# Optimization experiments

Measured on AMD Instinct MI355X. Metric: run time of the kernel, lower is better.

The kernel has to match this reference:

```python
import jax, jax.numpy as jnp
import numpy as np

EPS = 1e-5
NH, NP = 12, 4  # heads, points per level


def _ln(x, g, b):
    m = x.mean(-1, keepdims=True)
    v = x.var(-1, keepdims=True)
    return (x - m) / jnp.sqrt(v + EPS) * g + b


def _bilinear(v, g, H_, W_):
    # v: [B, nh, H_*W_, d] flattened feature map; g: [B, nh, Lq, np, 2] normalized locs in [0,1]
    # torch grid_sample(align_corners=False, padding='zeros') with grid = 2*loc-1 => pixel = loc*W - 0.5
    x = g[..., 0] * W_ - 0.5
    y = g[..., 1] * H_ - 0.5
    x0 = jnp.floor(x)
    y0 = jnp.floor(y)
    wx1 = x - x0
    wy1 = y - y0
    wx0 = 1.0 - wx1
    wy0 = 1.0 - wy1
    d = v.shape[-1]
    Bn, nh, Lq, np_ = x.shape
    out = jnp.zeros((Bn, nh, Lq, np_, d), v.dtype)
    for xi, yi, w in ((x0, y0, wx0 * wy0), (x0 + 1, y0, wx1 * wy0),
                      (x0, y0 + 1, wx0 * wy1), (x0 + 1, y0 + 1, wx1 * wy1)):
        valid = (xi >= 0) & (xi < W_) & (yi >= 0) & (yi < H_)
        xc = jnp.clip(xi, 0, W_ - 1).astype(jnp.int32)
        yc = jnp.clip(yi, 0, H_ - 1).astype(jnp.int32)
        idx = (yc * W_ + xc).reshape(Bn, nh, Lq * np_, 1)
        gv = jnp.take_along_axis(v, idx, axis=2).reshape(Bn, nh, Lq, np_, d)
        out = out + (w * valid.astype(v.dtype))[..., None] * gv
    return out


def setup_inputs() -> dict:
    key = jax.random.key(0)
    ks = jax.random.split(key, 16)
    B, Lq, C = 4, 4096, 768
    nl = 1
    Hs = Ws = 64
    Lin = Hs * Ws
    hid = int(C * 0.25)
    s = 0.02
    f32 = jnp.float32
    return {
        'query': jax.random.normal(ks[0], (B, Lq, C), f32),
        'reference_points': jax.random.uniform(ks[1], (B, Lq, nl, 2), f32),
        'feat': jax.random.normal(ks[2], (B, Lin, C), f32),
        'spatial_shapes': np.array([[Hs, Ws]], dtype=np.int64),
        'level_start_index': np.array([0], dtype=np.int64),
        'H': Hs, 'W': Ws,
        'qn_g': jnp.ones(C, f32), 'qn_b': jnp.zeros(C, f32),
        'fn_g': jnp.ones(C, f32), 'fn_b': jnp.zeros(C, f32),
        'Wv': jax.random.normal(ks[3], (C, C), f32) * s, 'bv': jnp.zeros(C, f32),
        'Woff': jax.random.normal(ks[4], (C, NH * nl * NP * 2), f32) * s,
        'boff': jax.random.normal(ks[5], (NH * nl * NP * 2,), f32) * 0.1,
        'Watt': jax.random.normal(ks[6], (C, NH * nl * NP), f32) * s,
        'batt': jnp.zeros(NH * nl * NP, f32),
        'Wout': jax.random.normal(ks[7], (C, C), f32) * s, 'bout': jnp.zeros(C, f32),
        'ffn_g': jnp.ones(C, f32), 'ffn_b': jnp.zeros(C, f32),
        'W1': jax.random.normal(ks[8], (C, hid), f32) * s, 'b1': jnp.zeros(hid, f32),
        'W2': jax.random.normal(ks[9], (hid, C), f32) * s, 'b2': jnp.zeros(C, f32),
    }


def reference(query, reference_points, feat, spatial_shapes, level_start_index, H, W,
              qn_g, qn_b, fn_g, fn_b, Wv, bv, Woff, boff, Watt, batt, Wout, bout,
              ffn_g, ffn_b, W1, b1, W2, b2):
    B, Lq, C = query.shape
    nl = spatial_shapes.shape[0]
    d = C // NH
    qn = _ln(query, qn_g, qn_b)
    fn = _ln(feat, fn_g, fn_b)
    value = (fn @ Wv + bv).reshape(B, -1, NH, d)
    off = (qn @ Woff + boff).reshape(B, Lq, NH, nl, NP, 2)
    attw = jax.nn.softmax((qn @ Watt + batt).reshape(B, Lq, NH, nl * NP), axis=-1)
    attw = attw.reshape(B, Lq, NH, nl, NP)
    # offset normalizer is [W_l, H_l]
    norm = np.stack([spatial_shapes[:, 1], spatial_shapes[:, 0]], -1).astype(np.float32)
    loc = reference_points[:, :, None, :, None, :] + off / jnp.asarray(norm)[None, None, None, :, None, :]
    out = jnp.zeros((B, NH, Lq, d), query.dtype)
    for l in range(nl):
        H_, W_ = int(spatial_shapes[l, 0]), int(spatial_shapes[l, 1])
        s0 = int(level_start_index[l])
        v = value[:, s0:s0 + H_ * W_].transpose(0, 2, 1, 3)       # [B, nh, HW, d]
        g = loc[:, :, :, l].transpose(0, 2, 1, 3, 4)              # [B, nh, Lq, np, 2]
        sampled = _bilinear(v, g, H_, W_)                         # [B, nh, Lq, np, d]
        w = attw[:, :, :, l].transpose(0, 2, 1, 3)                # [B, nh, Lq, np]
        out = out + jnp.sum(sampled * w[..., None], axis=3)
    attn = out.transpose(0, 2, 1, 3).reshape(B, Lq, C) @ Wout + bout
    query = query + attn
    h = _ln(query, ffn_g, ffn_b)
    h = jax.nn.gelu(h @ W1 + b1, approximate=False)
    return query + (h @ W2 + b2)
```

## Files before the change

kernel.cpp:

```cpp
#include <hip/hip_runtime.h>
#include <hip/hip_bf16.h>
#include <math.h>

#define B_    4
#define LQ    4096
#define CC    768
#define NH_   12
#define DH    64
#define NP_   4
#define HH    64
#define WW    64
#define HID   192
#define ROWS  (B_ * LQ)
#define EPS_  1e-5f

typedef __bf16 bf16x8 __attribute__((ext_vector_type(8)));
typedef __bf16 bf16x4 __attribute__((ext_vector_type(4)));
typedef float  f32x4  __attribute__((ext_vector_type(4)));

typedef __attribute__((address_space(3))) void* lds_vp;
typedef const __attribute__((address_space(1))) void* gbl_vp;

struct PrepJob { const float* W; __bf16* Wt; int K; int N; int Npad; };
struct PrepJobs { PrepJob j[6]; };

__global__ __launch_bounds__(256)
void prep_all(PrepJobs jobs) {
    PrepJob job = jobs.j[blockIdx.z];
    int k0 = blockIdx.x * 64, n0 = blockIdx.y * 64;
    if (k0 >= job.K || n0 >= job.Npad) return;
    __shared__ float tile[64][65];
    int c = threadIdx.x & 63, r0 = threadIdx.x >> 6;
    #pragma unroll
    for (int i = 0; i < 16; ++i) {
        int kk = i * 4 + r0;
        float v = 0.f;
        if (k0 + kk < job.K && n0 + c < job.N) v = job.W[(size_t)(k0 + kk) * job.N + n0 + c];
        tile[kk][c] = v;
    }
    __syncthreads();
    #pragma unroll
    for (int i = 0; i < 16; ++i) {
        int nn = i * 4 + r0;
        if (n0 + nn < job.Npad && k0 + c < job.K)
            job.Wt[(size_t)(n0 + nn) * job.K + k0 + c] = (__bf16)tile[c][nn];
    }
}

__inline__ __device__ float wave_sum64(float v) {
    #pragma unroll
    for (int o = 32; o > 0; o >>= 1) v += __shfl_down(v, o, 64);
    return v;
}

__global__ __launch_bounds__(256)
void ln2_kernel(const float* __restrict__ x0, const float* __restrict__ g0,
                const float* __restrict__ b0, __bf16* __restrict__ y0,
                const float* __restrict__ x1, const float* __restrict__ g1,
                const float* __restrict__ b1, __bf16* __restrict__ y1) {
    int sel = blockIdx.y;
    const float* x = sel ? x1 : x0;
    const float* g = sel ? g1 : g0;
    const float* b = sel ? b1 : b0;
    __bf16* y = sel ? y1 : y0;
    int row = blockIdx.x;
    const float* xr = x + (size_t)row * CC;
    __bf16* yr = y + (size_t)row * CC;
    int t = threadIdx.x;
    f32x4 xv = {0.f, 0.f, 0.f, 0.f};
    if (t < 192) xv = *(const f32x4*)(xr + t * 4);
    float s  = xv[0] + xv[1] + xv[2] + xv[3];
    float s2 = xv[0]*xv[0] + xv[1]*xv[1] + xv[2]*xv[2] + xv[3]*xv[3];
    __shared__ float red[8];
    float ws = wave_sum64(s), ws2 = wave_sum64(s2);
    int w = t >> 6;
    if ((t & 63) == 0) { red[w] = ws; red[4 + w] = ws2; }
    __syncthreads();
    float S  = red[0] + red[1] + red[2] + red[3];
    float S2 = red[4] + red[5] + red[6] + red[7];
    float mean = S / CC;
    float inv  = rsqrtf(S2 / CC - mean * mean + EPS_);
    if (t < 192) {
        f32x4 gv = *(const f32x4*)(g + t * 4);
        f32x4 bv = *(const f32x4*)(b + t * 4);
        bf16x4 o;
        #pragma unroll
        for (int e = 0; e < 4; ++e)
            o[e] = (__bf16)((xv[e] - mean) * inv * gv[e] + bv[e]);
        *(bf16x4*)(yr + t * 4) = o;
    }
}

__global__ __launch_bounds__(256)
void ln_bf_kernel(const __bf16* __restrict__ x, const float* __restrict__ g,
                  const float* __restrict__ b, __bf16* __restrict__ y) {
    int row = blockIdx.x;
    const __bf16* xr = x + (size_t)row * CC;
    __bf16* yr = y + (size_t)row * CC;
    int t = threadIdx.x;
    float xv[8]; bf16x8 raw = {};
    if (t < 96) raw = *(const bf16x8*)(xr + t * 8);
    float s = 0.f, s2 = 0.f;
    #pragma unroll
    for (int e = 0; e < 8; ++e) { xv[e] = (float)raw[e]; s += xv[e]; s2 += xv[e]*xv[e]; }
    __shared__ float red[8];
    float ws = wave_sum64(s), ws2 = wave_sum64(s2);
    int w = t >> 6;
    if ((t & 63) == 0) { red[w] = ws; red[4 + w] = ws2; }
    __syncthreads();
    float S  = red[0] + red[1] + red[2] + red[3];
    float S2 = red[4] + red[5] + red[6] + red[7];
    float mean = S / CC;
    float inv  = rsqrtf(S2 / CC - mean * mean + EPS_);
    if (t < 96) {
        bf16x8 o;
        #pragma unroll
        for (int e = 0; e < 8; ++e)
            o[e] = (__bf16)((xv[e] - mean) * inv * g[t * 8 + e] + b[t * 8 + e]);
        *(bf16x8*)(yr + t * 8) = o;
    }
}

__global__ __launch_bounds__(256)
void gemm_bt(const __bf16* __restrict__ A, const __bf16* __restrict__ Bt,
             const float* __restrict__ ba, int Nsplit, const float* __restrict__ bb,
             const void* __restrict__ res, void* __restrict__ out,
             int M, int K, int N, int flags) {
    __shared__ __bf16 As[128 * 32];
    __shared__ __bf16 Bs[128 * 32];

    int t = threadIdx.x;
    int lane = t & 63, wave = t >> 6;
    int bm = blockIdx.y * 128, bn = blockIdx.x * 128;
    int wm = wave & 1, wn = wave >> 1;

    f32x4 acc[4][4] = {};

    int row0 = t >> 2,           kc0 = (t & 3) ^ ((row0 >> 1) & 3);
    int row1 = (256 + t) >> 2,   kc1 = ((256 + t) & 3) ^ ((row1 >> 1) & 3);

    const __bf16* a0 = A  + (size_t)(bm + row0) * K + kc0 * 8;
    const __bf16* a1 = A  + (size_t)(bm + row1) * K + kc1 * 8;
    const __bf16* b0 = Bt + (size_t)(bn + row0) * K + kc0 * 8;
    const __bf16* b1 = Bt + (size_t)(bn + row1) * K + kc1 * 8;

    int rbase = wm * 64 + (lane & 15);
    int nbase = wn * 64 + (lane & 15);
    int kq = lane >> 4;

    for (int k0 = 0; k0 < K; k0 += 32) {
        __syncthreads();
        __builtin_amdgcn_global_load_lds((gbl_vp)(a0 + k0), (lds_vp)&As[t * 8], 16, 0, 0);
        __builtin_amdgcn_global_load_lds((gbl_vp)(a1 + k0), (lds_vp)&As[(256 + t) * 8], 16, 0, 0);
        __builtin_amdgcn_global_load_lds((gbl_vp)(b0 + k0), (lds_vp)&Bs[t * 8], 16, 0, 0);
        __builtin_amdgcn_global_load_lds((gbl_vp)(b1 + k0), (lds_vp)&Bs[(256 + t) * 8], 16, 0, 0);
        __syncthreads();

        bf16x8 afr[4], bfr[4];
        #pragma unroll
        for (int i = 0; i < 4; ++i) {
            int r = rbase + i * 16;
            afr[i] = *(const bf16x8*)&As[r * 32 + ((kq ^ ((r >> 1) & 3)) * 8)];
        }
        #pragma unroll
        for (int j = 0; j < 4; ++j) {
            int n = nbase + j * 16;
            bfr[j] = *(const bf16x8*)&Bs[n * 32 + ((kq ^ ((n >> 1) & 3)) * 8)];
        }
        #pragma unroll
        for (int i = 0; i < 4; ++i)
            #pragma unroll
            for (int j = 0; j < 4; ++j)
                acc[i][j] = __builtin_amdgcn_mfma_f32_16x16x32_bf16(afr[i], bfr[j], acc[i][j], 0, 0, 0);
    }

    int rowq = lane >> 4;
    int colj[4]; float biasj[4];
    #pragma unroll
    for (int j = 0; j < 4; ++j) {
        int c = bn + wn * 64 + j * 16 + (lane & 15);
        colj[j] = c;
        biasj[j] = (c < N) ? ((c < Nsplit) ? ba[c] : bb[c - Nsplit]) : 0.f;
    }
    int do_gelu = flags & 1, out_bf = flags & 2, res_bf = flags & 4;
    #pragma unroll
    for (int i = 0; i < 4; ++i) {
        #pragma unroll
        for (int r = 0; r < 4; ++r) {
            int m = bm + wm * 64 + i * 16 + rowq * 4 + r;
            #pragma unroll
            for (int j = 0; j < 4; ++j) {
                if (colj[j] < N) {
                    float v = acc[i][j][r] + biasj[j];
                    if (do_gelu) v = 0.5f * v * (1.f + erff(v * 0.70710678118f));
                    size_t oi = (size_t)m * N + colj[j];
                    if (res) v += res_bf ? (float)((const __bf16*)res)[oi]
                                         : ((const float*)res)[oi];
                    if (out_bf) ((__bf16*)out)[oi] = (__bf16)v;
                    else        ((float*)out)[oi]  = v;
                }
            }
        }
    }
}

__global__ __launch_bounds__(256)
void gemm_bt64(const __bf16* __restrict__ A, const __bf16* __restrict__ Bt,
               const float* __restrict__ ba, int Nsplit, const float* __restrict__ bb,
               void* __restrict__ out, int M, int K, int N, int flags) {
    __shared__ __bf16 As[64 * 32];
    __shared__ __bf16 Bs[64 * 32];

    int t = threadIdx.x;
    int lane = t & 63, wave = t >> 6;
    int bm = blockIdx.y * 64, bn = blockIdx.x * 64;

    f32x4 acc[4] = {};

    int row0 = t >> 2, kc0 = (t & 3) ^ ((row0 >> 1) & 3);
    const __bf16* a0 = A  + (size_t)(bm + row0) * K + kc0 * 8;
    const __bf16* b0 = Bt + (size_t)(bn + row0) * K + kc0 * 8;

    int rbase = wave * 16 + (lane & 15);
    int nbase = lane & 15;
    int kq = lane >> 4;

    for (int k0 = 0; k0 < K; k0 += 32) {
        __syncthreads();
        __builtin_amdgcn_global_load_lds((gbl_vp)(a0 + k0), (lds_vp)&As[t * 8], 16, 0, 0);
        __builtin_amdgcn_global_load_lds((gbl_vp)(b0 + k0), (lds_vp)&Bs[t * 8], 16, 0, 0);
        __syncthreads();

        bf16x8 afr = *(const bf16x8*)&As[rbase * 32 + ((kq ^ ((rbase >> 1) & 3)) * 8)];
        #pragma unroll
        for (int j = 0; j < 4; ++j) {
            int n = nbase + j * 16;
            bf16x8 bfr = *(const bf16x8*)&Bs[n * 32 + ((kq ^ ((n >> 1) & 3)) * 8)];
            acc[j] = __builtin_amdgcn_mfma_f32_16x16x32_bf16(afr, bfr, acc[j], 0, 0, 0);
        }
    }

    int rowq = lane >> 4;
    int do_gelu = flags & 1, out_bf = flags & 2;
    #pragma unroll
    for (int r = 0; r < 4; ++r) {
        int m = bm + wave * 16 + rowq * 4 + r;
        #pragma unroll
        for (int j = 0; j < 4; ++j) {
            int c = bn + j * 16 + (lane & 15);
            if (c < N) {
                float v = acc[j][r] + ((c < Nsplit) ? ba[c] : bb[c - Nsplit]);
                if (do_gelu) v = 0.5f * v * (1.f + erff(v * 0.70710678118f));
                size_t oi = (size_t)m * N + c;
                if (out_bf) ((__bf16*)out)[oi] = (__bf16)v;
                else        ((float*)out)[oi]  = v;
            }
        }
    }
}

__global__ __launch_bounds__(256)
void sample_kernel(const __bf16* __restrict__ value, const float* __restrict__ offatt,
                   const float* __restrict__ refp, __bf16* __restrict__ out) {
    int wid  = blockIdx.x * 4 + (threadIdx.x >> 6);
    int lane = threadIdx.x & 63;
    int h  = wid % NH_;
    int bq = wid / NH_;
    int b  = bq / LQ;

    const float* oa = offatt + (size_t)bq * 144;
    float rx = refp[(size_t)bq * 2 + 0] * (float)WW - 0.5f;
    float ry = refp[(size_t)bq * 2 + 1] * (float)HH - 0.5f;

    float l0 = oa[96 + h * 4 + 0], l1 = oa[96 + h * 4 + 1];
    float l2 = oa[96 + h * 4 + 2], l3 = oa[96 + h * 4 + 3];
    float mx = fmaxf(fmaxf(l0, l1), fmaxf(l2, l3));
    float e0 = __expf(l0 - mx), e1 = __expf(l1 - mx);
    float e2 = __expf(l2 - mx), e3 = __expf(l3 - mx);
    float rs = 1.f / (e0 + e1 + e2 + e3);

    int pp = lane >> 4;
    int g  = lane & 15;
    float wpl = (pp == 0) ? e0 : (pp == 1) ? e1 : (pp == 2) ? e2 : e3;
    wpl *= rs;

    const float* oxy = oa + h * 8 + pp * 2;
    float x = rx + oxy[0];
    float y = ry + oxy[1];
    float x0f = floorf(x), y0f = floorf(y);
    float wx1 = x - x0f, wy1 = y - y0f;
    float wx0 = 1.f - wx1, wy0 = 1.f - wy1;
    int x0 = (int)x0f, y0 = (int)y0f;
    int x1 = x0 + 1, y1 = y0 + 1;
    float mx0 = ((unsigned)x0 < (unsigned)WW) ? wx0 : 0.f;
    float mx1 = ((unsigned)x1 < (unsigned)WW) ? wx1 : 0.f;
    float my0 = (((unsigned)y0 < (unsigned)HH) ? wy0 : 0.f) * wpl;
    float my1 = (((unsigned)y1 < (unsigned)HH) ? wy1 : 0.f) * wpl;
    int xc0 = x0 & (WW - 1), xc1 = x1 & (WW - 1);
    int r0 = (y0 & (HH - 1)) << 6, r1 = (y1 & (HH - 1)) << 6;

    const __bf16* vbase = value + (size_t)b * (LQ * CC) + h * DH + g * 4;
    bf16x4 v00 = *(const bf16x4*)(vbase + (size_t)(r0 + xc0) * CC);
    bf16x4 v01 = *(const bf16x4*)(vbase + (size_t)(r0 + xc1) * CC);
    bf16x4 v10 = *(const bf16x4*)(vbase + (size_t)(r1 + xc0) * CC);
    bf16x4 v11 = *(const bf16x4*)(vbase + (size_t)(r1 + xc1) * CC);
    float w00 = mx0 * my0, w01 = mx1 * my0, w10 = mx0 * my1, w11 = mx1 * my1;

    f32x4 acc;
    #pragma unroll
    for (int e = 0; e < 4; ++e)
        acc[e] = w00 * (float)v00[e] + w01 * (float)v01[e]
               + w10 * (float)v10[e] + w11 * (float)v11[e];

    #pragma unroll
    for (int e = 0; e < 4; ++e) {
        acc[e] += __shfl_xor(acc[e], 16, 64);
        acc[e] += __shfl_xor(acc[e], 32, 64);
    }
    if (pp == 0) {
        bf16x4 o;
        o[0] = (__bf16)acc[0]; o[1] = (__bf16)acc[1];
        o[2] = (__bf16)acc[2]; o[3] = (__bf16)acc[3];
        *(bf16x4*)(out + (size_t)bq * CC + h * DH + g * 4) = o;
    }
}

extern "C" void kernel_launch(void* const* d_in, const int* in_sizes, int n_in,
                              void* d_out, int out_size, void* d_ws, size_t ws_size,
                              hipStream_t stream) {
    const float* query = (const float*)d_in[0];
    const float* refp  = (const float*)d_in[1];
    const float* feat  = (const float*)d_in[2];
    const float* qn_g  = (const float*)d_in[7];
    const float* qn_b  = (const float*)d_in[8];
    const float* fn_g  = (const float*)d_in[9];
    const float* fn_b  = (const float*)d_in[10];
    const float* Wv    = (const float*)d_in[11];
    const float* bv    = (const float*)d_in[12];
    const float* Woff  = (const float*)d_in[13];
    const float* boff  = (const float*)d_in[14];
    const float* Watt  = (const float*)d_in[15];
    const float* batt  = (const float*)d_in[16];
    const float* Wout  = (const float*)d_in[17];
    const float* bout  = (const float*)d_in[18];
    const float* ffn_g = (const float*)d_in[19];
    const float* ffn_b = (const float*)d_in[20];
    const float* W1    = (const float*)d_in[21];
    const float* b1    = (const float*)d_in[22];
    const float* W2    = (const float*)d_in[23];
    const float* b2    = (const float*)d_in[24];
    float* out = (float*)d_out;

    char* ws = (char*)d_ws;
    __bf16* WvT    = (__bf16*)(ws + 0);
    __bf16* WcombT = (__bf16*)(ws + 1179648);
    __bf16* WoutT  = (__bf16*)(ws + 1572864);
    __bf16* W1T    = (__bf16*)(ws + 2752512);
    __bf16* W2T    = (__bf16*)(ws + 3145728);
    float*  offatt_f = (float*)(ws + 3670016);
    __bf16* h1_bf    = (__bf16*)offatt_f;
    __bf16* bufA     = (__bf16*)(ws + 13107200);
    __bf16* qn_bf    = bufA;
    __bf16* value_bf = bufA;
    __bf16* bufB     = (__bf16*)(ws + 38273024);
    __bf16* fn_bf    = bufB;
    __bf16* samp_bf  = bufB;
    __bf16* h_bf     = bufB;
    __bf16* attn_bf  = (__bf16*)(ws + 63438848);

    dim3 blk(256);

    PrepJobs jobs;
    jobs.j[0] = {Wv,   WvT,             768, 768, 768};
    jobs.j[1] = {Woff, WcombT,          768,  96,  96};
    jobs.j[2] = {Watt, WcombT + 96*768, 768,  48,  96};
    jobs.j[3] = {Wout, WoutT,           768, 768, 768};
    jobs.j[4] = {W1,   W1T,             768, 192, 192};
    jobs.j[5] = {W2,   W2T,             192, 768, 768};
    prep_all<<<dim3(12, 12, 6), blk, 0, stream>>>(jobs);

    ln2_kernel<<<dim3(ROWS, 2), blk, 0, stream>>>(query, qn_g, qn_b, qn_bf,
                                                  feat,  fn_g, fn_b, fn_bf);

    gemm_bt64<<<dim3(3, ROWS / 64), blk, 0, stream>>>(
        qn_bf, WcombT, boff, 96, batt, offatt_f, ROWS, CC, 144, 0);
    gemm_bt<<<dim3(6, ROWS / 128), blk, 0, stream>>>(
        fn_bf, WvT, bv, CC, nullptr, nullptr, value_bf, ROWS, CC, CC, 2);
    sample_kernel<<<ROWS * NH_ / 4, blk, 0, stream>>>(value_bf, offatt_f, refp, samp_bf);
    gemm_bt<<<dim3(6, ROWS / 128), blk, 0, stream>>>(
        samp_bf, WoutT, bout, CC, nullptr, query, attn_bf, ROWS, CC, CC, 2);
    ln_bf_kernel<<<ROWS, blk, 0, stream>>>(attn_bf, ffn_g, ffn_b, h_bf);
    gemm_bt64<<<dim3(3, ROWS / 64), blk, 0, stream>>>(
        h_bf, W1T, b1, HID, nullptr, h1_bf, ROWS, CC, HID, 1 | 2);
    gemm_bt<<<dim3(6, ROWS / 128), blk, 0, stream>>>(
        h1_bf, W2T, b2, CC, nullptr, attn_bf, out, ROWS, HID, CC, 4);
}
```

Measured before the change: 451.3 us.

## Triple-buffer GEMM LDS tiles with async prefetch and swizzle block order

```diff
diff --git a/kernel.cpp b/kernel.cpp
--- a/kernel.cpp
+++ b/kernel.cpp
@@ -126,12 +126,19 @@
              const float* __restrict__ ba, int Nsplit, const float* __restrict__ bb,
              const void* __restrict__ res, void* __restrict__ out,
              int M, int K, int N, int flags) {
-    __shared__ __bf16 As[128 * 32];
-    __shared__ __bf16 Bs[128 * 32];
+    __shared__ __bf16 As[3][128 * 32];
+    __shared__ __bf16 Bs[3][128 * 32];
 
     int t = threadIdx.x;
     int lane = t & 63, wave = t >> 6;
-    int bm = blockIdx.y * 128, bn = blockIdx.x * 128;
+
+    int nwg = gridDim.x * gridDim.y;
+    int bid = blockIdx.y * gridDim.x + blockIdx.x;
+    int cpx = nwg >> 3;
+    int swz = (bid & 7) * cpx + (bid >> 3);
+    int bx = swz % gridDim.x, by = swz / gridDim.x;
+    int bm = by * 128, bn = bx * 128;
+
     int wm = wave & 1, wn = wave >> 1;
 
     f32x4 acc[4][4] = {};
@@ -148,31 +155,54 @@
     int nbase = wn * 64 + (lane & 15);
     int kq = lane >> 4;
 
-    for (int k0 = 0; k0 < K; k0 += 32) {
-        __syncthreads();
-        __builtin_amdgcn_global_load_lds((gbl_vp)(a0 + k0), (lds_vp)&As[t * 8], 16, 0, 0);
-        __builtin_amdgcn_global_load_lds((gbl_vp)(a1 + k0), (lds_vp)&As[(256 + t) * 8], 16, 0, 0);
-        __builtin_amdgcn_global_load_lds((gbl_vp)(b0 + k0), (lds_vp)&Bs[t * 8], 16, 0, 0);
-        __builtin_amdgcn_global_load_lds((gbl_vp)(b1 + k0), (lds_vp)&Bs[(256 + t) * 8], 16, 0, 0);
-        __syncthreads();
-
-        bf16x8 afr[4], bfr[4];
-        #pragma unroll
-        for (int i = 0; i < 4; ++i) {
-            int r = rbase + i * 16;
-            afr[i] = *(const bf16x8*)&As[r * 32 + ((kq ^ ((r >> 1) & 3)) * 8)];
-        }
-        #pragma unroll
-        for (int j = 0; j < 4; ++j) {
-            int n = nbase + j * 16;
-            bfr[j] = *(const bf16x8*)&Bs[n * 32 + ((kq ^ ((n >> 1) & 3)) * 8)];
-        }
-        #pragma unroll
-        for (int i = 0; i < 4; ++i)
-            #pragma unroll
-            for (int j = 0; j < 4; ++j)
-                acc[i][j] = __builtin_amdgcn_mfma_f32_16x16x32_bf16(afr[i], bfr[j], acc[i][j], 0, 0, 0);
-    }
+    #define STAGE128(bi, kt) do {                                                              \
+        int koff_ = (kt) * 32;                                                                 \
+        __builtin_amdgcn_global_load_lds((gbl_vp)(a0 + koff_), (lds_vp)&As[bi][t * 8], 16, 0, 0);         \
+        __builtin_amdgcn_global_load_lds((gbl_vp)(a1 + koff_), (lds_vp)&As[bi][(256 + t) * 8], 16, 0, 0); \
+        __builtin_amdgcn_global_load_lds((gbl_vp)(b0 + koff_), (lds_vp)&Bs[bi][t * 8], 16, 0, 0);         \
+        __builtin_amdgcn_global_load_lds((gbl_vp)(b1 + koff_), (lds_vp)&Bs[bi][(256 + t) * 8], 16, 0, 0); \
+    } while (0)
+
+    #define COMPUTE128(bi) do {                                                                \
+        bf16x8 afr[4], bfr[4];                                                                 \
+        _Pragma("unroll")                                                                      \
+        for (int i = 0; i < 4; ++i) {                                                          \
+            int r = rbase + i * 16;                                                            \
+            afr[i] = *(const bf16x8*)&As[bi][r * 32 + ((kq ^ ((r >> 1) & 3)) * 8)];            \
+        }                                                                                      \
+        _Pragma("unroll")                                                                      \
+        for (int j = 0; j < 4; ++j) {                                                          \
+            int n = nbase + j * 16;                                                            \
+            bfr[j] = *(const bf16x8*)&Bs[bi][n * 32 + ((kq ^ ((n >> 1) & 3)) * 8)];            \
+        }                                                                                      \
+        _Pragma("unroll")                                                                      \
+        for (int i = 0; i < 4; ++i)                                                            \
+            _Pragma("unroll")                                                                  \
+            for (int j = 0; j < 4; ++j)                                                        \
+                acc[i][j] = __builtin_amdgcn_mfma_f32_16x16x32_bf16(afr[i], bfr[j], acc[i][j], 0, 0, 0); \
+    } while (0)
+
+    int nt = K >> 5;
+    STAGE128(0, 0);
+    STAGE128(1, 1);
+    int bi = 0;
+    for (int tt = 0; tt < nt - 2; ++tt) {
+        int bnxt = bi + 2; if (bnxt >= 3) bnxt -= 3;
+        STAGE128(bnxt, tt + 2);
+        asm volatile("s_waitcnt vmcnt(8)\n\ts_barrier" ::: "memory");
+        COMPUTE128(bi);
+        asm volatile("s_barrier" ::: "memory");
+        ++bi; if (bi >= 3) bi -= 3;
+    }
+    asm volatile("s_waitcnt vmcnt(4)\n\ts_barrier" ::: "memory");
+    COMPUTE128(bi);
+    asm volatile("s_barrier" ::: "memory");
+    ++bi; if (bi >= 3) bi -= 3;
+    asm volatile("s_waitcnt vmcnt(0)\n\ts_barrier" ::: "memory");
+    COMPUTE128(bi);
+
+    #undef STAGE128
+    #undef COMPUTE128
 
     int rowq = lane >> 4;
     int colj[4]; float biasj[4];
@@ -208,12 +238,18 @@
 void gemm_bt64(const __bf16* __restrict__ A, const __bf16* __restrict__ Bt,
                const float* __restrict__ ba, int Nsplit, const float* __restrict__ bb,
                void* __restrict__ out, int M, int K, int N, int flags) {
-    __shared__ __bf16 As[64 * 32];
-    __shared__ __bf16 Bs[64 * 32];
+    __shared__ __bf16 As[3][64 * 32];
+    __shared__ __bf16 Bs[3][64 * 32];
 
     int t = threadIdx.x;
     int lane = t & 63, wave = t >> 6;
-    int bm = blockIdx.y * 64, bn = blockIdx.x * 64;
+
+    int nwg = gridDim.x * gridDim.y;
+    int bid = blockIdx.y * gridDim.x + blockIdx.x;
+    int cpx = nwg >> 3;
+    int swz = (bid & 7) * cpx + (bid >> 3);
+    int bx = swz % gridDim.x, by = swz / gridDim.x;
+    int bm = by * 64, bn = bx * 64;
 
     f32x4 acc[4] = {};
 
@@ -225,20 +261,43 @@
     int nbase = lane & 15;
     int kq = lane >> 4;
 
-    for (int k0 = 0; k0 < K; k0 += 32) {
-        __syncthreads();
-        __builtin_amdgcn_global_load_lds((gbl_vp)(a0 + k0), (lds_vp)&As[t * 8], 16, 0, 0);
-        __builtin_amdgcn_global_load_lds((gbl_vp)(b0 + k0), (lds_vp)&Bs[t * 8], 16, 0, 0);
-        __syncthreads();
-
-        bf16x8 afr = *(const bf16x8*)&As[rbase * 32 + ((kq ^ ((rbase >> 1) & 3)) * 8)];
-        #pragma unroll
-        for (int j = 0; j < 4; ++j) {
-            int n = nbase + j * 16;
-            bf16x8 bfr = *(const bf16x8*)&Bs[n * 32 + ((kq ^ ((n >> 1) & 3)) * 8)];
-            acc[j] = __builtin_amdgcn_mfma_f32_16x16x32_bf16(afr, bfr, acc[j], 0, 0, 0);
-        }
-    }
+    #define STAGE64(bi, kt) do {                                                               \
+        int koff_ = (kt) * 32;                                                                 \
+        __builtin_amdgcn_global_load_lds((gbl_vp)(a0 + koff_), (lds_vp)&As[bi][t * 8], 16, 0, 0); \
+        __builtin_amdgcn_global_load_lds((gbl_vp)(b0 + koff_), (lds_vp)&Bs[bi][t * 8], 16, 0, 0); \
+    } while (0)
+
+    #define COMPUTE64(bi) do {                                                                 \
+        bf16x8 afr = *(const bf16x8*)&As[bi][rbase * 32 + ((kq ^ ((rbase >> 1) & 3)) * 8)];    \
+        _Pragma("unroll")                                                                      \
+        for (int j = 0; j < 4; ++j) {                                                          \
+            int n = nbase + j * 16;                                                            \
+            bf16x8 bfr = *(const bf16x8*)&Bs[bi][n * 32 + ((kq ^ ((n >> 1) & 3)) * 8)];        \
+            acc[j] = __builtin_amdgcn_mfma_f32_16x16x32_bf16(afr, bfr, acc[j], 0, 0, 0);       \
+        }                                                                                      \
+    } while (0)
+
+    int nt = K >> 5;
+    STAGE64(0, 0);
+    STAGE64(1, 1);
+    int bi = 0;
+    for (int tt = 0; tt < nt - 2; ++tt) {
+        int bnxt = bi + 2; if (bnxt >= 3) bnxt -= 3;
+        STAGE64(bnxt, tt + 2);
+        asm volatile("s_waitcnt vmcnt(4)\n\ts_barrier" ::: "memory");
+        COMPUTE64(bi);
+        asm volatile("s_barrier" ::: "memory");
+        ++bi; if (bi >= 3) bi -= 3;
+    }
+    asm volatile("s_waitcnt vmcnt(2)\n\ts_barrier" ::: "memory");
+    COMPUTE64(bi);
+    asm volatile("s_barrier" ::: "memory");
+    ++bi; if (bi >= 3) bi -= 3;
+    asm volatile("s_waitcnt vmcnt(0)\n\ts_barrier" ::: "memory");
+    COMPUTE64(bi);
+
+    #undef STAGE64
+    #undef COMPUTE64
 
     int rowq = lane >> 4;
     int do_gelu = flags & 1, out_bf = flags & 2;
```

Measured after the change: 438.0 us. 2.9% less time.

## Unify GEMMs into double-buffered 64x64 kernel with block swizzle

Applied to the files above, without the earlier changes.

```diff
diff --git a/kernel.cpp b/kernel.cpp
--- a/kernel.cpp
+++ b/kernel.cpp
@@ -121,99 +121,22 @@
     }
 }
 
-__global__ __launch_bounds__(256)
-void gemm_bt(const __bf16* __restrict__ A, const __bf16* __restrict__ Bt,
-             const float* __restrict__ ba, int Nsplit, const float* __restrict__ bb,
-             const void* __restrict__ res, void* __restrict__ out,
-             int M, int K, int N, int flags) {
-    __shared__ __bf16 As[128 * 32];
-    __shared__ __bf16 Bs[128 * 32];
+__global__ __launch_bounds__(256, 8)
+void gemm64(const __bf16* __restrict__ A, const __bf16* __restrict__ Bt,
+            const float* __restrict__ ba, int Nsplit, const float* __restrict__ bb,
+            const void* __restrict__ res, void* __restrict__ out,
+            int M, int K, int N, int flags) {
+    __shared__ __bf16 As[2][64 * 32];
+    __shared__ __bf16 Bs[2][64 * 32];
 
     int t = threadIdx.x;
     int lane = t & 63, wave = t >> 6;
-    int bm = blockIdx.y * 128, bn = blockIdx.x * 128;
-    int wm = wave & 1, wn = wave >> 1;
-
-    f32x4 acc[4][4] = {};
-
-    int row0 = t >> 2,           kc0 = (t & 3) ^ ((row0 >> 1) & 3);
-    int row1 = (256 + t) >> 2,   kc1 = ((256 + t) & 3) ^ ((row1 >> 1) & 3);
-
-    const __bf16* a0 = A  + (size_t)(bm + row0) * K + kc0 * 8;
-    const __bf16* a1 = A  + (size_t)(bm + row1) * K + kc1 * 8;
-    const __bf16* b0 = Bt + (size_t)(bn + row0) * K + kc0 * 8;
-    const __bf16* b1 = Bt + (size_t)(bn + row1) * K + kc1 * 8;
-
-    int rbase = wm * 64 + (lane & 15);
-    int nbase = wn * 64 + (lane & 15);
-    int kq = lane >> 4;
-
-    for (int k0 = 0; k0 < K; k0 += 32) {
-        __syncthreads();
-        __builtin_amdgcn_global_load_lds((gbl_vp)(a0 + k0), (lds_vp)&As[t * 8], 16, 0, 0);
-        __builtin_amdgcn_global_load_lds((gbl_vp)(a1 + k0), (lds_vp)&As[(256 + t) * 8], 16, 0, 0);
-        __builtin_amdgcn_global_load_lds((gbl_vp)(b0 + k0), (lds_vp)&Bs[t * 8], 16, 0, 0);
-        __builtin_amdgcn_global_load_lds((gbl_vp)(b1 + k0), (lds_vp)&Bs[(256 + t) * 8], 16, 0, 0);
-        __syncthreads();
-
-        bf16x8 afr[4], bfr[4];
-        #pragma unroll
-        for (int i = 0; i < 4; ++i) {
-            int r = rbase + i * 16;
-            afr[i] = *(const bf16x8*)&As[r * 32 + ((kq ^ ((r >> 1) & 3)) * 8)];
-        }
-        #pragma unroll
-        for (int j = 0; j < 4; ++j) {
-            int n = nbase + j * 16;
-            bfr[j] = *(const bf16x8*)&Bs[n * 32 + ((kq ^ ((n >> 1) & 3)) * 8)];
-        }
-        #pragma unroll
-        for (int i = 0; i < 4; ++i)
-            #pragma unroll
-            for (int j = 0; j < 4; ++j)
-                acc[i][j] = __builtin_amdgcn_mfma_f32_16x16x32_bf16(afr[i], bfr[j], acc[i][j], 0, 0, 0);
-    }
-
-    int rowq = lane >> 4;
-    int colj[4]; float biasj[4];
-    #pragma unroll
-    for (int j = 0; j < 4; ++j) {
-        int c = bn + wn * 64 + j * 16 + (lane & 15);
-        colj[j] = c;
-        biasj[j] = (c < N) ? ((c < Nsplit) ? ba[c] : bb[c - Nsplit]) : 0.f;
-    }
-    int do_gelu = flags & 1, out_bf = flags & 2, res_bf = flags & 4;
-    #pragma unroll
-    for (int i = 0; i < 4; ++i) {
-        #pragma unroll
-        for (int r = 0; r < 4; ++r) {
-            int m = bm + wm * 64 + i * 16 + rowq * 4 + r;
-            #pragma unroll
-            for (int j = 0; j < 4; ++j) {
-                if (colj[j] < N) {
-                    float v = acc[i][j][r] + biasj[j];
-                    if (do_gelu) v = 0.5f * v * (1.f + erff(v * 0.70710678118f));
-                    size_t oi = (size_t)m * N + colj[j];
-                    if (res) v += res_bf ? (float)((const __bf16*)res)[oi]
-                                         : ((const float*)res)[oi];
-                    if (out_bf) ((__bf16*)out)[oi] = (__bf16)v;
-                    else        ((float*)out)[oi]  = v;
-                }
-            }
-        }
-    }
-}
-
-__global__ __launch_bounds__(256)
-void gemm_bt64(const __bf16* __restrict__ A, const __bf16* __restrict__ Bt,
-               const float* __restrict__ ba, int Nsplit, const float* __restrict__ bb,
-               void* __restrict__ out, int M, int K, int N, int flags) {
-    __shared__ __bf16 As[64 * 32];
-    __shared__ __bf16 Bs[64 * 32];
-
-    int t = threadIdx.x;
-    int lane = t & 63, wave = t >> 6;
-    int bm = blockIdx.y * 64, bn = blockIdx.x * 64;
+
+    int nwg = gridDim.x * gridDim.y;
+    int bid = blockIdx.y * gridDim.x + blockIdx.x;
+    int swz = (bid & 7) * (nwg >> 3) + (bid >> 3);
+    int bx = swz % gridDim.x, by = swz / gridDim.x;
+    int bm = by * 64, bn = bx * 64;
 
     f32x4 acc[4] = {};
 
@@ -225,33 +148,52 @@
     int nbase = lane & 15;
     int kq = lane >> 4;
 
-    for (int k0 = 0; k0 < K; k0 += 32) {
-        __syncthreads();
-        __builtin_amdgcn_global_load_lds((gbl_vp)(a0 + k0), (lds_vp)&As[t * 8], 16, 0, 0);
-        __builtin_amdgcn_global_load_lds((gbl_vp)(b0 + k0), (lds_vp)&Bs[t * 8], 16, 0, 0);
-        __syncthreads();
-
-        bf16x8 afr = *(const bf16x8*)&As[rbase * 32 + ((kq ^ ((rbase >> 1) & 3)) * 8)];
-        #pragma unroll
-        for (int j = 0; j < 4; ++j) {
-            int n = nbase + j * 16;
-            bf16x8 bfr = *(const bf16x8*)&Bs[n * 32 + ((kq ^ ((n >> 1) & 3)) * 8)];
-            acc[j] = __builtin_amdgcn_mfma_f32_16x16x32_bf16(afr, bfr, acc[j], 0, 0, 0);
-        }
-    }
+    #define STAGE(bi, kt) do {                                                                   \
+        int koff_ = (kt) * 32;                                                                   \
+        __builtin_amdgcn_global_load_lds((gbl_vp)(a0 + koff_), (lds_vp)&As[bi][t * 8], 16, 0, 0); \
+        __builtin_amdgcn_global_load_lds((gbl_vp)(b0 + koff_), (lds_vp)&Bs[bi][t * 8], 16, 0, 0); \
+    } while (0)
+
+    #define COMPUTE(bi) do {                                                                     \
+        bf16x8 afr = *(const bf16x8*)&As[bi][rbase * 32 + ((kq ^ ((rbase >> 1) & 3)) * 8)];      \
+        _Pragma("unroll")                                                                        \
+        for (int j = 0; j < 4; ++j) {                                                            \
+            int n = nbase + j * 16;                                                              \
+            bf16x8 bfr = *(const bf16x8*)&Bs[bi][n * 32 + ((kq ^ ((n >> 1) & 3)) * 8)];          \
+            acc[j] = __builtin_amdgcn_mfma_f32_16x16x32_bf16(afr, bfr, acc[j], 0, 0, 0);         \
+        }                                                                                        \
+    } while (0)
+
+    int nt = K >> 5;
+    STAGE(0, 0);
+    STAGE(1, 1);
+    for (int tt = 0; tt < nt; ++tt) {
+        int cur = tt & 1;
+        if (tt < nt - 1) asm volatile("s_waitcnt vmcnt(2)\n\ts_barrier" ::: "memory");
+        else             asm volatile("s_waitcnt vmcnt(0)\n\ts_barrier" ::: "memory");
+        COMPUTE(cur);
+        asm volatile("s_waitcnt lgkmcnt(0)\n\ts_barrier" ::: "memory");
+        if (tt + 2 < nt) STAGE(cur, tt + 2);
+    }
+
+    #undef STAGE
+    #undef COMPUTE
 
     int rowq = lane >> 4;
-    int do_gelu = flags & 1, out_bf = flags & 2;
-    #pragma unroll
-    for (int r = 0; r < 4; ++r) {
-        int m = bm + wave * 16 + rowq * 4 + r;
-        #pragma unroll
-        for (int j = 0; j < 4; ++j) {
-            int c = bn + j * 16 + (lane & 15);
-            if (c < N) {
-                float v = acc[j][r] + ((c < Nsplit) ? ba[c] : bb[c - Nsplit]);
+    int do_gelu = flags & 1, out_bf = flags & 2, res_bf = flags & 4;
+    #pragma unroll
+    for (int j = 0; j < 4; ++j) {
+        int c = bn + j * 16 + (lane & 15);
+        if (c < N) {
+            float bias = (c < Nsplit) ? ba[c] : bb[c - Nsplit];
+            #pragma unroll
+            for (int r = 0; r < 4; ++r) {
+                int m = bm + wave * 16 + rowq * 4 + r;
+                float v = acc[j][r] + bias;
                 if (do_gelu) v = 0.5f * v * (1.f + erff(v * 0.70710678118f));
                 size_t oi = (size_t)m * N + c;
+                if (res) v += res_bf ? (float)((const __bf16*)res)[oi]
+                                     : ((const float*)res)[oi];
                 if (out_bf) ((__bf16*)out)[oi] = (__bf16)v;
                 else        ((float*)out)[oi]  = v;
             }
@@ -382,16 +324,16 @@
     ln2_kernel<<<dim3(ROWS, 2), blk, 0, stream>>>(query, qn_g, qn_b, qn_bf,
                                                   feat,  fn_g, fn_b, fn_bf);
 
-    gemm_bt64<<<dim3(3, ROWS / 64), blk, 0, stream>>>(
-        qn_bf, WcombT, boff, 96, batt, offatt_f, ROWS, CC, 144, 0);
-    gemm_bt<<<dim3(6, ROWS / 128), blk, 0, stream>>>(
+    gemm64<<<dim3(3, ROWS / 64), blk, 0, stream>>>(
+        qn_bf, WcombT, boff, 96, batt, nullptr, offatt_f, ROWS, CC, 144, 0);
+    gemm64<<<dim3(12, ROWS / 64), blk, 0, stream>>>(
         fn_bf, WvT, bv, CC, nullptr, nullptr, value_bf, ROWS, CC, CC, 2);
     sample_kernel<<<ROWS * NH_ / 4, blk, 0, stream>>>(value_bf, offatt_f, refp, samp_bf);
-    gemm_bt<<<dim3(6, ROWS / 128), blk, 0, stream>>>(
+    gemm64<<<dim3(12, ROWS / 64), blk, 0, stream>>>(
         samp_bf, WoutT, bout, CC, nullptr, query, attn_bf, ROWS, CC, CC, 2);
     ln_bf_kernel<<<ROWS, blk, 0, stream>>>(attn_bf, ffn_g, ffn_b, h_bf);
-    gemm_bt64<<<dim3(3, ROWS / 64), blk, 0, stream>>>(
-        h_bf, W1T, b1, HID, nullptr, h1_bf, ROWS, CC, HID, 1 | 2);
-    gemm_bt<<<dim3(6, ROWS / 128), blk, 0, stream>>>(
+    gemm64<<<dim3(3, ROWS / 64), blk, 0, stream>>>(
+        h_bf, W1T, b1, HID, nullptr, nullptr, h1_bf, ROWS, CC, HID, 1 | 2);
+    gemm64<<<dim3(12, ROWS / 64), blk, 0, stream>>>(
         h1_bf, W2T, b2, CC, nullptr, attn_bf, out, ROWS, HID, CC, 4);
 }
```

Result: faster. 431.4 us (-4.4%).
